# Performance work log

Hardware: AMD Instinct MI355X
Metric: run time of the kernel (lower is better)

## Reference

```python
import jax, jax.numpy as jnp
import numpy as np

N, E, G = 100000, 400000, 2000
D = 128            # dim_node
DE = 128 + 300     # dim_edge after RBF concat
NC = 300           # RBF centers
CUT_LO, CUT_HI = 0.0, 30.0
N_CONV = 3


def setup_inputs() -> dict:
    key = jax.random.key(0)
    ks = jax.random.split(key, 32)
    inp = {}
    inp['Z'] = jax.random.randint(ks[0], (N,), 0, 20)
    inp['edge_type'] = jax.random.randint(ks[1], (E,), 0, 400)
    inp['dist'] = jax.random.uniform(ks[2], (E,), dtype=jnp.float32) * CUT_HI
    inp['src'] = jax.random.randint(ks[3], (E,), 0, N)
    inp['dst'] = jax.random.randint(ks[4], (E,), 0, N)
    inp['graph_ids'] = jnp.sort(jax.random.randint(ks[5], (N,), 0, G))
    s = 0.05
    inp['node_emb'] = jax.random.normal(ks[6], (20, D), jnp.float32) * s
    inp['edge_emb'] = jax.random.normal(ks[7], (400, D), jnp.float32) * s
    # per-conv-layer weights, stacked over layer dim
    inp['Wn1'] = jax.random.normal(ks[8], (N_CONV, D, D), jnp.float32) * s
    inp['bn1'] = jnp.zeros((N_CONV, D), jnp.float32)
    inp['Wn2'] = jax.random.normal(ks[9], (N_CONV, D, D), jnp.float32) * s
    inp['bn2'] = jnp.zeros((N_CONV, D), jnp.float32)
    inp['We1'] = jax.random.normal(ks[10], (N_CONV, DE, DE), jnp.float32) * s
    inp['be1'] = jnp.zeros((N_CONV, DE), jnp.float32)
    inp['We2'] = jax.random.normal(ks[11], (N_CONV, D, DE), jnp.float32) * s
    inp['be2'] = jnp.zeros((N_CONV, D), jnp.float32)
    inp['Wc'] = jax.random.normal(ks[12], (N_CONV, D, D), jnp.float32) * s
    inp['bc'] = jnp.zeros((N_CONV, D), jnp.float32)
    # read layer
    inp['Wr1'] = jax.random.normal(ks[13], (D, D), jnp.float32) * s
    inp['br1'] = jnp.zeros((D,), jnp.float32)
    inp['Wr2'] = jax.random.normal(ks[14], (1, D), jnp.float32) * s
    inp['br2'] = jnp.zeros((1,), jnp.float32)
    return inp


def _rbf(dist):
    centers = jnp.linspace(CUT_LO, CUT_HI, NC, dtype=jnp.float32)
    gap = centers[1] - centers[0]
    # [E, NC]
    return jnp.exp(-((dist[:, None] - centers[None, :]) ** 2) / gap)


def reference(Z, edge_type, dist, src, dst, graph_ids,
              node_emb, edge_emb,
              Wn1, bn1, Wn2, bn2, We1, be1, We2, be2, Wc, bc,
              Wr1, br1, Wr2, br2):
    h = node_emb[Z]                          # [N, D] node embedding
    e = edge_emb[edge_type]                  # [E, D] edge embedding
    e = jnp.concatenate([e, _rbf(dist)], axis=1)   # [E, DE]
    for i in range(N_CONV):
        hs = h[src]                          # gather src node feats [E, D]
        hn = jax.nn.relu(hs @ Wn1[i].T + bn1[i]) @ Wn2[i].T + bn2[i]   # [E, D]
        ee = jax.nn.relu(e @ We1[i].T + be1[i]) @ We2[i].T + be2[i]    # [E, D]
        m = jnp.tanh((hn * ee) @ Wc[i].T + bc[i])                      # [E, D]
        h = h + jax.ops.segment_sum(m, dst, num_segments=N)            # scatter-sum
    r = jax.nn.relu(h @ Wr1.T + br1) @ Wr2.T + br2                     # [N, 1]
    out = jax.ops.segment_sum(r, graph_ids, num_segments=G)            # [G, 1]
    return out.flatten()                                               # [G]
```

## Files before the change

kernel.cpp:

```cpp
#include <hip/hip_runtime.h>

#define NN 100000
#define En 400000
#define Gn 2000
#define GRID 2048

typedef unsigned short u16;
typedef unsigned int u32;
typedef _Float16 f16;
typedef f16 f16x8 __attribute__((ext_vector_type(8)));
typedef float f32x4 __attribute__((ext_vector_type(4)));

__device__ __forceinline__ void lds_barrier() {
  asm volatile("s_waitcnt lgkmcnt(0)\ns_barrier" ::: "memory");
}

#define MFMA16(a, b, c) __builtin_amdgcn_mfma_f32_16x16x32_f16(a, b, c, 0, 0, 0)


__global__ __launch_bounds__(256) void k_prepw(
    const float* __restrict__ Wn1, const float* __restrict__ Wn2,
    const float* __restrict__ Wc, const float* __restrict__ We2,
    const float* __restrict__ We1,
    f16* __restrict__ Wn1b, f16* __restrict__ Wn2b, f16* __restrict__ Wcb,
    f16* __restrict__ We2b, f16* __restrict__ Rb) {
  int i = blockIdx.x * 256 + threadIdx.x;
  if (i < 49152) {
    Wn1b[i] = (f16)Wn1[i];
  } else if (i < 98304) {
    int j = i - 49152;
    Wn2b[j] = (f16)Wn2[j];
  } else if (i < 147456) {
    int j = i - 98304;
    Wcb[j] = (f16)Wc[j];
  } else if (i < 319488) {
    int j = i - 147456;
    int l = j / 57344;
    int r = j - l * 57344;
    int row = r / 448;
    int k = r - row * 448;
    float v = (k < 428) ? We2[l * 54784 + row * 428 + k] : 0.f;
    We2b[j] = (f16)v;
  } else if (i < 749568) {
    int j = i - 319488;
    int l = j / 143360;
    int r = j - l * 143360;
    int row = r / 320;
    int k = r - row * 320;
    float v = 0.f;
    if (row < 428 && k < 300) v = We1[(size_t)l * 183184 + row * 428 + 128 + k];
    Rb[j] = (f16)v;
  }
}


__global__ __launch_bounds__(256) void k_t2(const float* __restrict__ edge_emb,
                                            const float* __restrict__ We1,
                                            const float* __restrict__ be1,
                                            f16* __restrict__ T2) {
  __shared__ __align__(16) float sWe[64][32 * 4];
  __shared__ float sB[64];
  const int tid = threadIdx.x;
  const int l = blockIdx.x / 28;
  const int rb = blockIdx.x - l * 28;
  const int jb = rb >> 2;
  const int tc = rb & 3;
  const int j0 = jb * 64;
  for (int idx = tid; idx < 64 * 32; idx += 256) {
    int row = idx >> 5, c = idx & 31;
    int gj = j0 + row;
    float4 v = make_float4(0.f, 0.f, 0.f, 0.f);
    if (gj < 428)
      v = *(const float4*)&We1[(size_t)l * 183184 + gj * 428 + c * 4];
    *(float4*)&sWe[row][c * 4] = v;
  }
  if (tid < 64) {
    int gj = j0 + tid;
    sB[tid] = (gj < 428) ? be1[l * 428 + gj] : 0.f;
  }
  lds_barrier();
  const int jl = tid & 63, tl = tid >> 6;
  const int gj = j0 + jl;
  for (int it = 0; it < 25; ++it) {
    int t = tc * 100 + it * 4 + tl;
    const float4* er = (const float4*)(edge_emb + t * 128);
    float s = 0.f;
#pragma unroll
    for (int d = 0; d < 32; ++d) {
      float4 a = er[d];
      float4 b = *(const float4*)&sWe[jl][d * 4];
      s += a.x * b.x + a.y * b.y + a.z * b.z + a.w * b.w;
    }
    s += sB[jl];
    T2[l * 179200 + t * 448 + gj] = (gj < 428) ? (f16)s : (f16)0.f;
  }
}

__global__ __launch_bounds__(256) void k_dtab(const f16* __restrict__ Rb,
                                              f16* __restrict__ Dtab) {
  const int tid = threadIdx.x;
  int l = blockIdx.x / (GRID + 1);
  int g = blockIdx.x - l * (GRID + 1);
  float d = (float)g * (30.f / (float)GRID);
  int kc = (int)(d * (299.f / 30.f) + 0.5f);
  int kk0 = min(max(kc - 16, 0), 268);
  __shared__ float sE[32];
  if (tid < 32) {
    float x = d - (float)(kk0 + tid) * (30.f / 299.f);
    sE[tid] = __expf(-x * x * (299.f / 30.f));
  }
  __syncthreads();
  for (int j = tid; j < 448; j += 256) {
    const f16* rr = &Rb[((size_t)l * 448 + j) * 320 + kk0];
    float s = 0.f;
#pragma unroll
    for (int k = 0; k < 32; ++k) s += sE[k] * (float)rr[k];
    Dtab[((size_t)(l * (GRID + 1) + g)) * 448 + j] = (f16)s;
  }
}


__global__ __launch_bounds__(256) void k_zero32(u32* __restrict__ p, int n) {
  int i = blockIdx.x * 256 + threadIdx.x;
  if (i < n) p[i] = 0u;
}

__global__ __launch_bounds__(256) void k_hist(const int* __restrict__ dstv,
                                              u32* __restrict__ hist) {
  int e = blockIdx.x * 256 + threadIdx.x;
  if (e < En) atomicAdd(&hist[dstv[e]], 1u);
}

__global__ __launch_bounds__(1024) void k_scan1(const u32* __restrict__ hist,
                                                u32* __restrict__ excl,
                                                u32* __restrict__ part) {
  __shared__ u32 s[1024];
  const int t = threadIdx.x, b = blockIdx.x, i = b * 1024 + t;
  u32 v = (i < NN) ? hist[i] : 0u;
  s[t] = v;
  __syncthreads();
  u32 acc = v;
  for (int off = 1; off < 1024; off <<= 1) {
    u32 add = (t >= off) ? s[t - off] : 0u;
    __syncthreads();
    acc += add;
    s[t] = acc;
    __syncthreads();
  }
  if (i < NN) excl[i] = acc - v;
  if (t == 1023) part[b] = acc;
}

__global__ __launch_bounds__(128) void k_scan2(u32* __restrict__ part, int n) {
  __shared__ u32 s[128];
  const int t = threadIdx.x;
  u32 v = (t < n) ? part[t] : 0u;
  s[t] = v;
  __syncthreads();
  u32 acc = v;
  for (int off = 1; off < 128; off <<= 1) {
    u32 add = (t >= off) ? s[t - off] : 0u;
    __syncthreads();
    acc += add;
    s[t] = acc;
    __syncthreads();
  }
  if (t < n) part[t] = acc - v;
}

__global__ __launch_bounds__(1024) void k_scan3(const u32* __restrict__ excl,
                                                const u32* __restrict__ part,
                                                u32* __restrict__ cursor) {
  int i = blockIdx.x * 1024 + threadIdx.x;
  if (i < NN) cursor[i] = excl[i] + part[blockIdx.x];
}

__global__ __launch_bounds__(256) void k_scatter(const int* __restrict__ etype,
                                                 const float* __restrict__ dist,
                                                 const int* __restrict__ srcv,
                                                 const int* __restrict__ dstv,
                                                 u32* __restrict__ cursor,
                                                 int4* __restrict__ epack,
                                                 int* __restrict__ edst) {
  int e = blockIdx.x * 256 + threadIdx.x;
  if (e >= En) return;
  int d = dstv[e];
  int pos = (int)atomicAdd(&cursor[d], 1u);
  float fi = dist[e] * ((float)GRID / 30.f);
  int ix = (int)fi;
  epack[pos] = make_int4(srcv[e], etype[e] * 448, ix * 448,
                         __float_as_int(fi - (float)ix));
  edst[pos] = d;
}


__global__ __launch_bounds__(256) void k_node(const float* __restrict__ h,
                                              const f16* __restrict__ W1,
                                              const float* __restrict__ b1,
                                              const f16* __restrict__ W2,
                                              const float* __restrict__ b2,
                                              f16* __restrict__ n2) {
  __shared__ __align__(16) f16 sH[64 * 136];
  __shared__ __align__(16) f16 sT[64 * 136];
  const int tid = threadIdx.x;
  const int nbase = blockIdx.x * 64;
  for (int i = tid; i < 64 * 128; i += 256) {
    int e = i >> 7, d = i & 127;
    int node = nbase + e;
    float v = (node < NN) ? h[(size_t)node * 128 + d] : 0.f;
    sH[e * 136 + d] = (f16)v;
  }
  lds_barrier();
  const int lane = tid & 63, wave = tid >> 6;
  const int q = lane >> 4, ln = lane & 15;
  const int nb = wave * 32;

  f32x4 acc[4][2];
#pragma unroll
  for (int m = 0; m < 4; ++m)
#pragma unroll
    for (int n = 0; n < 2; ++n) acc[m][n] = 0.f;
#pragma unroll
  for (int k0 = 0; k0 < 128; k0 += 32) {
    f16x8 a[4];
#pragma unroll
    for (int m = 0; m < 4; ++m)
      a[m] = *(const f16x8*)&sH[(m * 16 + ln) * 136 + k0 + q * 8];
#pragma unroll
    for (int n = 0; n < 2; ++n) {
      f16x8 b = *(const f16x8*)&W1[(nb + n * 16 + ln) * 128 + k0 + q * 8];
#pragma unroll
      for (int m = 0; m < 4; ++m) acc[m][n] = MFMA16(a[m], b, acc[m][n]);
    }
  }
#pragma unroll
  for (int n = 0; n < 2; ++n) {
    int col = nb + n * 16 + ln;
    float bb = b1[col];
#pragma unroll
    for (int m = 0; m < 4; ++m)
#pragma unroll
      for (int r = 0; r < 4; ++r) {
        int row = m * 16 + q * 4 + r;
        sT[row * 136 + col] = (f16)fmaxf(acc[m][n][r] + bb, 0.f);
      }
  }
  lds_barrier();

  f32x4 acc2[4][2];
#pragma unroll
  for (int m = 0; m < 4; ++m)
#pragma unroll
    for (int n = 0; n < 2; ++n) acc2[m][n] = 0.f;
#pragma unroll
  for (int k0 = 0; k0 < 128; k0 += 32) {
    f16x8 a[4];
#pragma unroll
    for (int m = 0; m < 4; ++m)
      a[m] = *(const f16x8*)&sT[(m * 16 + ln) * 136 + k0 + q * 8];
#pragma unroll
    for (int n = 0; n < 2; ++n) {
      f16x8 b = *(const f16x8*)&W2[(nb + n * 16 + ln) * 128 + k0 + q * 8];
#pragma unroll
      for (int m = 0; m < 4; ++m) acc2[m][n] = MFMA16(a[m], b, acc2[m][n]);
    }
  }
#pragma unroll
  for (int n = 0; n < 2; ++n) {
    int col = nb + n * 16 + ln;
    float bb = b2[col];
#pragma unroll
    for (int m = 0; m < 4; ++m)
#pragma unroll
      for (int r = 0; r < 4; ++r) {
        int row = m * 16 + q * 4 + r;
        int node = nbase + row;
        if (node < NN) n2[(size_t)node * 128 + col] = (f16)(acc2[m][n][r] + bb);
      }
  }
}


__global__ __launch_bounds__(256) void k_node0(const int* __restrict__ Z,
                                               const float* __restrict__ node_emb,
                                               const f16* __restrict__ W1,
                                               const float* __restrict__ b1,
                                               const f16* __restrict__ W2,
                                               const float* __restrict__ b2,
                                               f16* __restrict__ n2,
                                               float* __restrict__ h,
                                               float* __restrict__ out) {
  __shared__ __align__(16) f16 sH[64 * 136];
  __shared__ __align__(16) f16 sT[64 * 136];
  __shared__ int sZ[64];
  const int tid = threadIdx.x;
  const int nbase = blockIdx.x * 64;
  {
    int oi = blockIdx.x * 256 + tid;
    if (oi < Gn) out[oi] = 0.f;
  }
  if (tid < 64) sZ[tid] = Z[min(nbase + tid, NN - 1)];
  lds_barrier();
  for (int i = tid; i < 64 * 128; i += 256) {
    int e = i >> 7, d = i & 127;
    int node = nbase + e;
    float v = node_emb[sZ[e] * 128 + d];
    sH[e * 136 + d] = (f16)v;
    if (node < NN) h[(size_t)node * 128 + d] = v;
  }
  lds_barrier();
  const int lane = tid & 63, wave = tid >> 6;
  const int q = lane >> 4, ln = lane & 15;
  const int nb = wave * 32;

  f32x4 acc[4][2];
#pragma unroll
  for (int m = 0; m < 4; ++m)
#pragma unroll
    for (int n = 0; n < 2; ++n) acc[m][n] = 0.f;
#pragma unroll
  for (int k0 = 0; k0 < 128; k0 += 32) {
    f16x8 a[4];
#pragma unroll
    for (int m = 0; m < 4; ++m)
      a[m] = *(const f16x8*)&sH[(m * 16 + ln) * 136 + k0 + q * 8];
#pragma unroll
    for (int n = 0; n < 2; ++n) {
      f16x8 b = *(const f16x8*)&W1[(nb + n * 16 + ln) * 128 + k0 + q * 8];
#pragma unroll
      for (int m = 0; m < 4; ++m) acc[m][n] = MFMA16(a[m], b, acc[m][n]);
    }
  }
#pragma unroll
  for (int n = 0; n < 2; ++n) {
    int col = nb + n * 16 + ln;
    float bb = b1[col];
#pragma unroll
    for (int m = 0; m < 4; ++m)
#pragma unroll
      for (int r = 0; r < 4; ++r) {
        int row = m * 16 + q * 4 + r;
        sT[row * 136 + col] = (f16)fmaxf(acc[m][n][r] + bb, 0.f);
      }
  }
  lds_barrier();

  f32x4 acc2[4][2];
#pragma unroll
  for (int m = 0; m < 4; ++m)
#pragma unroll
    for (int n = 0; n < 2; ++n) acc2[m][n] = 0.f;
#pragma unroll
  for (int k0 = 0; k0 < 128; k0 += 32) {
    f16x8 a[4];
#pragma unroll
    for (int m = 0; m < 4; ++m)
      a[m] = *(const f16x8*)&sT[(m * 16 + ln) * 136 + k0 + q * 8];
#pragma unroll
    for (int n = 0; n < 2; ++n) {
      f16x8 b = *(const f16x8*)&W2[(nb + n * 16 + ln) * 128 + k0 + q * 8];
#pragma unroll
      for (int m = 0; m < 4; ++m) acc2[m][n] = MFMA16(a[m], b, acc2[m][n]);
    }
  }
#pragma unroll
  for (int n = 0; n < 2; ++n) {
    int col = nb + n * 16 + ln;
    float bb = b2[col];
#pragma unroll
    for (int m = 0; m < 4; ++m)
#pragma unroll
      for (int r = 0; r < 4; ++r) {
        int row = m * 16 + q * 4 + r;
        int node = nbase + row;
        if (node < NN) n2[(size_t)node * 128 + col] = (f16)(acc2[m][n][r] + bb);
      }
  }
}


__global__ __launch_bounds__(256)
__attribute__((amdgpu_waves_per_eu(4, 4))) void k_edge(
    const int4* __restrict__ epack, const int* __restrict__ edst,
    const f16* __restrict__ T2, const f16* __restrict__ Dtab,
    const f16* __restrict__ We2b, const float* __restrict__ be2,
    const f16* __restrict__ Wcb, const float* __restrict__ bc,
    const f16* __restrict__ n2, float* __restrict__ h) {
  __shared__ __align__(16) f16 sC[2][64 * 136];
  __shared__ int sSrc[64], sDst[64], sT2o[64], sIdx[64];
  __shared__ float sFrac[64];

  const int tid = threadIdx.x;
  const int e0 = blockIdx.x * 64;
  if (tid < 64) {
    int4 p = epack[e0 + tid];
    sSrc[tid] = p.x;
    sT2o[tid] = p.y;
    sIdx[tid] = p.z;
    sFrac[tid] = __int_as_float(p.w);
    sDst[tid] = edst[e0 + tid];
  }
  lds_barrier();

  const int lane = tid & 63, wave = tid >> 6;
  const int q = lane >> 4, ln = lane & 15;
  const int nb = wave * 32;

  f32x4 acc[4][2];
#pragma unroll
  for (int m = 0; m < 4; ++m)
#pragma unroll
    for (int n = 0; n < 2; ++n) acc[m][n] = 0.f;

  auto lerp_relu = [](f16x8 lo, f16x8 hi, f16x8 t2, f16 fr) -> f16x8 {
    f16x8 v = t2 + lo + (hi - lo) * fr;
    f16x8 z = {};
    return __builtin_elementwise_max(v, z);
  };
  auto pf128 = [&](int k0, f16x8* plo, f16x8* phi, f16x8* pt2, f16* pfr) {
    const int cg = tid & 15, eb = tid >> 4;
    const int col = k0 + cg * 8;
#pragma unroll
    for (int i = 0; i < 4; ++i) {
      int e = eb + i * 16;
      int off = sIdx[e] + col;
      plo[i] = *(const f16x8*)&Dtab[off];
      phi[i] = *(const f16x8*)&Dtab[off + 448];
      pt2[i] = *(const f16x8*)&T2[sT2o[e] + col];
      pfr[i] = (f16)sFrac[e];
    }
  };
  auto st128 = [&](f16* buf, const f16x8* plo, const f16x8* phi,
                   const f16x8* pt2, const f16* pfr) {
    const int cg = tid & 15, eb = tid >> 4;
#pragma unroll
    for (int i = 0; i < 4; ++i) {
      int e = eb + i * 16;
      *(f16x8*)&buf[e * 136 + cg * 8] = lerp_relu(plo[i], phi[i], pt2[i], pfr[i]);
    }
  };
  auto pf64 = [&](f16x8* plo, f16x8* phi, f16x8* pt2, f16* pfr) {
    const int cg = tid & 7, eb = tid >> 3;
    const int col = 384 + cg * 8;
#pragma unroll
    for (int i = 0; i < 2; ++i) {
      int e = eb + i * 32;
      int off = sIdx[e] + col;
      plo[i] = *(const f16x8*)&Dtab[off];
      phi[i] = *(const f16x8*)&Dtab[off + 448];
      pt2[i] = *(const f16x8*)&T2[sT2o[e] + col];
      pfr[i] = (f16)sFrac[e];
    }
  };
  auto st64 = [&](f16* buf, const f16x8* plo, const f16x8* phi,
                  const f16x8* pt2, const f16* pfr) {
    const int cg = tid & 7, eb = tid >> 3;
#pragma unroll
    for (int i = 0; i < 2; ++i) {
      int e = eb + i * 32;
      *(f16x8*)&buf[e * 136 + cg * 8] = lerp_relu(plo[i], phi[i], pt2[i], pfr[i]);
    }
  };
  auto mfma_chunk = [&](const f16* buf, int k0, int nk) {
    for (int kk = 0; kk < nk; ++kk) {
      f16x8 a[4];
#pragma unroll
      for (int m = 0; m < 4; ++m)
        a[m] = *(const f16x8*)&buf[(m * 16 + ln) * 136 + kk * 32 + q * 8];
#pragma unroll
      for (int n = 0; n < 2; ++n) {
        f16x8 b = *(const f16x8*)&We2b[(nb + n * 16 + ln) * 448 + k0 + kk * 32 + q * 8];
#pragma unroll
        for (int m = 0; m < 4; ++m) acc[m][n] = MFMA16(a[m], b, acc[m][n]);
      }
    }
  };

  {
    f16x8 plo[4], phi[4], pt2[4]; f16 pfr[4];
    pf128(0, plo, phi, pt2, pfr);
    st128(sC[0], plo, phi, pt2, pfr);
  }
  lds_barrier();
  {
    f16x8 plo[4], phi[4], pt2[4]; f16 pfr[4];
    pf128(128, plo, phi, pt2, pfr);
    mfma_chunk(sC[0], 0, 4);
    st128(sC[1], plo, phi, pt2, pfr);
  }
  lds_barrier();
  {
    f16x8 plo[4], phi[4], pt2[4]; f16 pfr[4];
    pf128(256, plo, phi, pt2, pfr);
    mfma_chunk(sC[1], 128, 4);
    st128(sC[0], plo, phi, pt2, pfr);
  }
  lds_barrier();
  f16x8 nrows[4];
  {
    f16x8 plo[2], phi[2], pt2[2]; f16 pfr[2];
    pf64(plo, phi, pt2, pfr);
#pragma unroll
    for (int i = 0; i < 4; ++i) {
      int u = tid + 256 * i;
      int e = u >> 4, cg = u & 15;
      nrows[i] = *(const f16x8*)&n2[(size_t)sSrc[e] * 128 + cg * 8];
    }
    mfma_chunk(sC[0], 256, 4);
    st64(sC[1], plo, phi, pt2, pfr);
  }
  lds_barrier();

  f16* sN = sC[0];
#pragma unroll
  for (int i = 0; i < 4; ++i) {
    int u = tid + 256 * i;
    int e = u >> 4, cg = u & 15;
    *(f16x8*)&sN[e * 136 + cg * 8] = nrows[i];
  }
  mfma_chunk(sC[1], 384, 2);
  lds_barrier();

  f16* sP = sC[1];
  {
    float be2v[2] = {be2[nb + ln], be2[nb + 16 + ln]};
#pragma unroll
    for (int n = 0; n < 2; ++n) {
      int col = nb + n * 16 + ln;
#pragma unroll
      for (int m = 0; m < 4; ++m)
#pragma unroll
        for (int r = 0; r < 4; ++r) {
          int row = m * 16 + q * 4 + r;
          float ee = acc[m][n][r] + be2v[n];
          sP[row * 136 + col] = (f16)(ee * (float)sN[row * 136 + col]);
        }
    }
  }
  lds_barrier();

  {
    f32x4 acc2[4][2];
#pragma unroll
    for (int m = 0; m < 4; ++m)
#pragma unroll
      for (int n = 0; n < 2; ++n) acc2[m][n] = 0.f;
#pragma unroll
    for (int k0 = 0; k0 < 128; k0 += 32) {
      f16x8 a[4];
#pragma unroll
      for (int m = 0; m < 4; ++m)
        a[m] = *(const f16x8*)&sP[(m * 16 + ln) * 136 + k0 + q * 8];
#pragma unroll
      for (int n = 0; n < 2; ++n) {
        f16x8 b = *(const f16x8*)&Wcb[(nb + n * 16 + ln) * 128 + k0 + q * 8];
#pragma unroll
        for (int m = 0; m < 4; ++m) acc2[m][n] = MFMA16(a[m], b, acc2[m][n]);
      }
    }
    float bcv[2] = {bc[nb + ln], bc[nb + 16 + ln]};
#pragma unroll
    for (int m = 0; m < 4; ++m) {
      int d[4];
#pragma unroll
      for (int r = 0; r < 4; ++r) d[r] = sDst[m * 16 + q * 4 + r];
#pragma unroll
      for (int n = 0; n < 2; ++n) {
        int col = nb + n * 16 + ln;
        float tv[4];
#pragma unroll
        for (int r = 0; r < 4; ++r) {
          float x = acc2[m][n][r] + bcv[n];
          x = fminf(2.f, fmaxf(-2.f, x));
          float x2 = x * x;
          tv[r] = x * (15.f + x2) * __builtin_amdgcn_rcpf(15.f + 6.f * x2);
        }
        float s = tv[0];
        int cur = d[0];
#pragma unroll
        for (int r = 1; r < 4; ++r) {
          if (d[r] == cur) {
            s += tv[r];
          } else {
            unsafeAtomicAdd(&h[(size_t)cur * 128 + col], s);
            cur = d[r];
            s = tv[r];
          }
        }
        unsafeAtomicAdd(&h[(size_t)cur * 128 + col], s);
      }
    }
  }
}


__global__ __launch_bounds__(256) void k_read(const float* __restrict__ h,
                                              const float* __restrict__ Wr1,
                                              const float* __restrict__ br1,
                                              const float* __restrict__ Wr2,
                                              const float* __restrict__ br2,
                                              const int* __restrict__ gid,
                                              float* __restrict__ out) {
  __shared__ __align__(16) f16 sH[64 * 136];
  __shared__ __align__(16) f16 sW[128 * 136];
  __shared__ float sR4[4][64];
  const int tid = threadIdx.x;
  const int nbase = blockIdx.x * 64;
  for (int i = tid; i < 64 * 128; i += 256) {
    int e = i >> 7, d = i & 127;
    int node = nbase + e;
    float v = (node < NN) ? h[(size_t)node * 128 + d] : 0.f;
    sH[e * 136 + d] = (f16)v;
  }
  for (int i = tid; i < 128 * 128; i += 256) {
    int rr = i >> 7, d = i & 127;
    sW[rr * 136 + d] = (f16)Wr1[i];
  }
  lds_barrier();
  const int lane = tid & 63, wave = tid >> 6;
  const int q = lane >> 4, ln = lane & 15;
  const int nb = wave * 32;

  f32x4 acc[4][2];
#pragma unroll
  for (int m = 0; m < 4; ++m)
#pragma unroll
    for (int n = 0; n < 2; ++n) acc[m][n] = 0.f;
#pragma unroll
  for (int k0 = 0; k0 < 128; k0 += 32) {
    f16x8 a[4];
#pragma unroll
    for (int m = 0; m < 4; ++m)
      a[m] = *(const f16x8*)&sH[(m * 16 + ln) * 136 + k0 + q * 8];
#pragma unroll
    for (int n = 0; n < 2; ++n) {
      f16x8 b = *(const f16x8*)&sW[(nb + n * 16 + ln) * 136 + k0 + q * 8];
#pragma unroll
      for (int m = 0; m < 4; ++m) acc[m][n] = MFMA16(a[m], b, acc[m][n]);
    }
  }
#pragma unroll
  for (int m = 0; m < 4; ++m)
#pragma unroll
    for (int r = 0; r < 4; ++r) {
      float t = 0.f;
#pragma unroll
      for (int n = 0; n < 2; ++n) {
        int col = nb + n * 16 + ln;
        t += fmaxf(acc[m][n][r] + br1[col], 0.f) * Wr2[col];
      }
      t += __shfl_xor(t, 1);
      t += __shfl_xor(t, 2);
      t += __shfl_xor(t, 4);
      t += __shfl_xor(t, 8);
      if (ln == 0) sR4[wave][m * 16 + q * 4 + r] = t;
    }
  lds_barrier();
  if (tid < 64) {
    int node = nbase + tid;
    if (node < NN) {
      float s = sR4[0][tid] + sR4[1][tid] + sR4[2][tid] + sR4[3][tid] + br2[0];
      unsafeAtomicAdd(&out[gid[node]], s);
    }
  }
}


extern "C" void kernel_launch(void* const* d_in, const int* in_sizes, int n_in,
                              void* d_out, int out_size, void* d_ws, size_t ws_size,
                              hipStream_t stream) {
  const int* Z = (const int*)d_in[0];
  const int* etype = (const int*)d_in[1];
  const float* dist = (const float*)d_in[2];
  const int* src = (const int*)d_in[3];
  const int* dst = (const int*)d_in[4];
  const int* gid = (const int*)d_in[5];
  const float* node_emb = (const float*)d_in[6];
  const float* edge_emb = (const float*)d_in[7];
  const float* Wn1 = (const float*)d_in[8];
  const float* bn1 = (const float*)d_in[9];
  const float* Wn2 = (const float*)d_in[10];
  const float* bn2 = (const float*)d_in[11];
  const float* We1 = (const float*)d_in[12];
  const float* be1 = (const float*)d_in[13];
  const float* We2 = (const float*)d_in[14];
  const float* be2 = (const float*)d_in[15];
  const float* Wc = (const float*)d_in[16];
  const float* bc = (const float*)d_in[17];
  const float* Wr1 = (const float*)d_in[18];
  const float* br1 = (const float*)d_in[19];
  const float* Wr2 = (const float*)d_in[20];
  const float* br2 = (const float*)d_in[21];
  float* out = (float*)d_out;

  char* ws = (char*)d_ws;
  float* h = (float*)(ws);
  f16* n2 = (f16*)(ws + 51200000);
  f16* Rb = (f16*)(ws + 76800000);
  f16* We2b = (f16*)(ws + 77660160);
  f16* Wcb = (f16*)(ws + 78004224);
  f16* Wn1b = (f16*)(ws + 78102528);
  f16* Wn2b = (f16*)(ws + 78200832);
  f16* T2 = (f16*)(ws + 78299136);
  f16* Dtab = (f16*)(ws + 79374336);
  int4* epack = (int4*)(ws + 84882048);
  int* edst = (int*)(ws + 91282048);
  u32* hist = (u32*)(ws + 92882048);
  u32* cursor = (u32*)(ws + 93282048);
  u32* excl = (u32*)(ws + 93682048);
  u32* part = (u32*)(ws + 94082048);

  k_zero32<<<391, 256, 0, stream>>>(hist, NN);
  k_hist<<<1563, 256, 0, stream>>>(dst, hist);
  k_scan1<<<98, 1024, 0, stream>>>(hist, excl, part);
  k_scan2<<<1, 128, 0, stream>>>(part, 98);
  k_scan3<<<98, 1024, 0, stream>>>(excl, part, cursor);
  k_scatter<<<1563, 256, 0, stream>>>(etype, dist, src, dst, cursor, epack, edst);

  k_prepw<<<2928, 256, 0, stream>>>(Wn1, Wn2, Wc, We2, We1,
                                    Wn1b, Wn2b, Wcb, We2b, Rb);
  k_t2<<<84, 256, 0, stream>>>(edge_emb, We1, be1, T2);
  k_dtab<<<3 * (GRID + 1), 256, 0, stream>>>(Rb, Dtab);

  for (int l = 0; l < 3; ++l) {
    if (l == 0) {
      k_node0<<<1563, 256, 0, stream>>>(Z, node_emb, Wn1b, bn1, Wn2b, bn2,
                                        n2, h, out);
    } else {
      k_node<<<1563, 256, 0, stream>>>(h, Wn1b + l * 16384, bn1 + l * 128,
                                       Wn2b + l * 16384, bn2 + l * 128, n2);
    }
    k_edge<<<6250, 256, 0, stream>>>(epack, edst,
                                     T2 + l * 179200, Dtab + (size_t)l * (GRID + 1) * 448,
                                     We2b + l * 57344, be2 + l * 128,
                                     Wcb + l * 16384, bc + l * 128, n2, h);
  }
  k_read<<<1563, 256, 0, stream>>>(h, Wr1, br1, Wr2, br2, gid, out);
}
```

Measured before the change: 943.0 us.

## Fold histogram zeroing into weight prep and tune several small kernels

Moves the histogram zeroing into the weight-conversion kernel, which removes one launch. Rewrites the edge-type table kernel to use MFMA tiles instead of scalar FP32 dot products. Replaces the LDS-based block scan with wave shuffles and vectorises the h/weight staging loads to float4. Widens the RBF window to 40 aligned taps with vector loads and raises wave priority around the MFMA loops in the edge kernel. The table values now go through FP16 matmul and a slightly different RBF truncation, so numerics shift a little.

```diff
diff --git a/kernel.cpp b/kernel.cpp
--- a/kernel.cpp
+++ b/kernel.cpp
@@ -9,6 +9,7 @@
 typedef unsigned int u32;
 typedef _Float16 f16;
 typedef f16 f16x8 __attribute__((ext_vector_type(8)));
+typedef f16 f16x4 __attribute__((ext_vector_type(4)));
 typedef float f32x4 __attribute__((ext_vector_type(4)));
 
 __device__ __forceinline__ void lds_barrier() {
@@ -23,7 +24,7 @@
     const float* __restrict__ Wc, const float* __restrict__ We2,
     const float* __restrict__ We1,
     f16* __restrict__ Wn1b, f16* __restrict__ Wn2b, f16* __restrict__ Wcb,
-    f16* __restrict__ We2b, f16* __restrict__ Rb) {
+    f16* __restrict__ We2b, f16* __restrict__ Rb, u32* __restrict__ hist) {
   int i = blockIdx.x * 256 + threadIdx.x;
   if (i < 49152) {
     Wn1b[i] = (f16)Wn1[i];
@@ -50,6 +51,8 @@
     float v = 0.f;
     if (row < 428 && k < 300) v = We1[(size_t)l * 183184 + row * 428 + 128 + k];
     Rb[j] = (f16)v;
+  } else if (i < 849568) {
+    hist[i - 749568] = 0u;
   }
 }
 
@@ -58,41 +61,68 @@
                                             const float* __restrict__ We1,
                                             const float* __restrict__ be1,
                                             f16* __restrict__ T2) {
-  __shared__ __align__(16) float sWe[64][32 * 4];
-  __shared__ float sB[64];
+  __shared__ __align__(16) f16 sA[64 * 136];
+  __shared__ __align__(16) f16 sB[128 * 136];
   const int tid = threadIdx.x;
   const int l = blockIdx.x / 28;
   const int rb = blockIdx.x - l * 28;
-  const int jb = rb >> 2;
-  const int tc = rb & 3;
-  const int j0 = jb * 64;
-  for (int idx = tid; idx < 64 * 32; idx += 256) {
-    int row = idx >> 5, c = idx & 31;
-    int gj = j0 + row;
+  const int tb = rb >> 2, jb = rb & 3;
+  const int t0 = tb * 64, j0 = jb * 128;
+  for (int i = tid; i < 64 * 32; i += 256) {
+    int e = i >> 5, c = (i & 31) * 4;
+    int t = t0 + e;
     float4 v = make_float4(0.f, 0.f, 0.f, 0.f);
-    if (gj < 428)
-      v = *(const float4*)&We1[(size_t)l * 183184 + gj * 428 + c * 4];
-    *(float4*)&sWe[row][c * 4] = v;
-  }
-  if (tid < 64) {
-    int gj = j0 + tid;
-    sB[tid] = (gj < 428) ? be1[l * 428 + gj] : 0.f;
-  }
-  lds_barrier();
-  const int jl = tid & 63, tl = tid >> 6;
-  const int gj = j0 + jl;
-  for (int it = 0; it < 25; ++it) {
-    int t = tc * 100 + it * 4 + tl;
-    const float4* er = (const float4*)(edge_emb + t * 128);
-    float s = 0.f;
-#pragma unroll
-    for (int d = 0; d < 32; ++d) {
-      float4 a = er[d];
-      float4 b = *(const float4*)&sWe[jl][d * 4];
-      s += a.x * b.x + a.y * b.y + a.z * b.z + a.w * b.w;
-    }
-    s += sB[jl];
-    T2[l * 179200 + t * 448 + gj] = (gj < 428) ? (f16)s : (f16)0.f;
+    if (t < 400) v = *(const float4*)&edge_emb[t * 128 + c];
+    f16x4 o = {(f16)v.x, (f16)v.y, (f16)v.z, (f16)v.w};
+    *(f16x4*)&sA[e * 136 + c] = o;
+  }
+  for (int i = tid; i < 128 * 32; i += 256) {
+    int rr = i >> 5, c = (i & 31) * 4;
+    int j = j0 + rr;
+    float4 v = make_float4(0.f, 0.f, 0.f, 0.f);
+    if (j < 428) v = *(const float4*)&We1[(size_t)l * 183184 + j * 428 + c];
+    f16x4 o = {(f16)v.x, (f16)v.y, (f16)v.z, (f16)v.w};
+    *(f16x4*)&sB[rr * 136 + c] = o;
+  }
+  lds_barrier();
+  const int lane = tid & 63, wave = tid >> 6;
+  const int q = lane >> 4, ln = lane & 15;
+  const int nb = wave * 32;
+
+  f32x4 acc[4][2];
+#pragma unroll
+  for (int m = 0; m < 4; ++m)
+#pragma unroll
+    for (int n = 0; n < 2; ++n) acc[m][n] = 0.f;
+#pragma unroll
+  for (int k0 = 0; k0 < 128; k0 += 32) {
+    f16x8 a[4];
+#pragma unroll
+    for (int m = 0; m < 4; ++m)
+      a[m] = *(const f16x8*)&sA[(m * 16 + ln) * 136 + k0 + q * 8];
+#pragma unroll
+    for (int n = 0; n < 2; ++n) {
+      f16x8 b = *(const f16x8*)&sB[(nb + n * 16 + ln) * 136 + k0 + q * 8];
+#pragma unroll
+      for (int m = 0; m < 4; ++m) acc[m][n] = MFMA16(a[m], b, acc[m][n]);
+    }
+  }
+#pragma unroll
+  for (int n = 0; n < 2; ++n) {
+    int col = nb + n * 16 + ln;
+    int gj = j0 + col;
+    float bb = (gj < 428) ? be1[l * 428 + gj] : 0.f;
+#pragma unroll
+    for (int m = 0; m < 4; ++m)
+#pragma unroll
+      for (int r = 0; r < 4; ++r) {
+        int row = m * 16 + q * 4 + r;
+        int t = t0 + row;
+        if (t < 400 && gj < 448) {
+          float s = acc[m][n][r] + bb;
+          T2[l * 179200 + t * 448 + gj] = (gj < 428) ? (f16)s : (f16)0.f;
+        }
+      }
   }
 }
 
@@ -103,9 +133,9 @@
   int g = blockIdx.x - l * (GRID + 1);
   float d = (float)g * (30.f / (float)GRID);
   int kc = (int)(d * (299.f / 30.f) + 0.5f);
-  int kk0 = min(max(kc - 16, 0), 268);
-  __shared__ float sE[32];
-  if (tid < 32) {
+  int kk0 = min(max(kc - 20, 0), 280) & ~7;
+  __shared__ float sE[40];
+  if (tid < 40) {
     float x = d - (float)(kk0 + tid) * (30.f / 299.f);
     sE[tid] = __expf(-x * x * (299.f / 30.f));
   }
@@ -114,16 +144,15 @@
     const f16* rr = &Rb[((size_t)l * 448 + j) * 320 + kk0];
     float s = 0.f;
 #pragma unroll
-    for (int k = 0; k < 32; ++k) s += sE[k] * (float)rr[k];
+    for (int v = 0; v < 5; ++v) {
+      f16x8 rv = *(const f16x8*)&rr[v * 8];
+#pragma unroll
+      for (int t = 0; t < 8; ++t) s += sE[v * 8 + t] * (float)rv[t];
+    }
     Dtab[((size_t)(l * (GRID + 1) + g)) * 448 + j] = (f16)s;
   }
 }
 
-
-__global__ __launch_bounds__(256) void k_zero32(u32* __restrict__ p, int n) {
-  int i = blockIdx.x * 256 + threadIdx.x;
-  if (i < n) p[i] = 0u;
-}
 
 __global__ __launch_bounds__(256) void k_hist(const int* __restrict__ dstv,
                                               u32* __restrict__ hist) {
@@ -134,21 +163,32 @@
 __global__ __launch_bounds__(1024) void k_scan1(const u32* __restrict__ hist,
                                                 u32* __restrict__ excl,
                                                 u32* __restrict__ part) {
-  __shared__ u32 s[1024];
+  __shared__ u32 ws[16];
   const int t = threadIdx.x, b = blockIdx.x, i = b * 1024 + t;
+  const int lane = t & 63, wid = t >> 6;
   u32 v = (i < NN) ? hist[i] : 0u;
-  s[t] = v;
+  u32 acc = v;
+#pragma unroll
+  for (int off = 1; off < 64; off <<= 1) {
+    u32 x = __shfl_up(acc, off);
+    if (lane >= off) acc += x;
+  }
+  if (lane == 63) ws[wid] = acc;
   __syncthreads();
-  u32 acc = v;
-  for (int off = 1; off < 1024; off <<= 1) {
-    u32 add = (t >= off) ? s[t - off] : 0u;
-    __syncthreads();
-    acc += add;
-    s[t] = acc;
-    __syncthreads();
-  }
-  if (i < NN) excl[i] = acc - v;
-  if (t == 1023) part[b] = acc;
+  if (t < 16) {
+    u32 wa = ws[t];
+#pragma unroll
+    for (int off = 1; off < 16; off <<= 1) {
+      u32 x = __shfl_up(wa, off);
+      if (t >= off) wa += x;
+    }
+    ws[t] = wa;
+  }
+  __syncthreads();
+  u32 base = (wid > 0) ? ws[wid - 1] : 0u;
+  u32 inc = base + acc;
+  if (i < NN) excl[i] = inc - v;
+  if (t == 1023) part[b] = inc;
 }
 
 __global__ __launch_bounds__(128) void k_scan2(u32* __restrict__ part, int n) {
@@ -204,11 +244,13 @@
   __shared__ __align__(16) f16 sT[64 * 136];
   const int tid = threadIdx.x;
   const int nbase = blockIdx.x * 64;
-  for (int i = tid; i < 64 * 128; i += 256) {
-    int e = i >> 7, d = i & 127;
+  for (int i = tid; i < 64 * 32; i += 256) {
+    int e = i >> 5, c = (i & 31) * 4;
     int node = nbase + e;
-    float v = (node < NN) ? h[(size_t)node * 128 + d] : 0.f;
-    sH[e * 136 + d] = (f16)v;
+    float4 v = make_float4(0.f, 0.f, 0.f, 0.f);
+    if (node < NN) v = *(const float4*)&h[(size_t)node * 128 + c];
+    f16x4 o = {(f16)v.x, (f16)v.y, (f16)v.z, (f16)v.w};
+    *(f16x4*)&sH[e * 136 + c] = o;
   }
   lds_barrier();
   const int lane = tid & 63, wave = tid >> 6;
@@ -301,12 +343,13 @@
   }
   if (tid < 64) sZ[tid] = Z[min(nbase + tid, NN - 1)];
   lds_barrier();
-  for (int i = tid; i < 64 * 128; i += 256) {
-    int e = i >> 7, d = i & 127;
+  for (int i = tid; i < 64 * 32; i += 256) {
+    int e = i >> 5, c = (i & 31) * 4;
     int node = nbase + e;
-    float v = node_emb[sZ[e] * 128 + d];
-    sH[e * 136 + d] = (f16)v;
-    if (node < NN) h[(size_t)node * 128 + d] = v;
+    float4 v = *(const float4*)&node_emb[sZ[e] * 128 + c];
+    f16x4 o = {(f16)v.x, (f16)v.y, (f16)v.z, (f16)v.w};
+    *(f16x4*)&sH[e * 136 + c] = o;
+    if (node < NN) *(float4*)&h[(size_t)node * 128 + c] = v;
   }
   lds_barrier();
   const int lane = tid & 63, wave = tid >> 6;
@@ -462,6 +505,7 @@
     }
   };
   auto mfma_chunk = [&](const f16* buf, int k0, int nk) {
+    __builtin_amdgcn_s_setprio(1);
     for (int kk = 0; kk < nk; ++kk) {
       f16x8 a[4];
 #pragma unroll
@@ -474,6 +518,7 @@
         for (int m = 0; m < 4; ++m) acc[m][n] = MFMA16(a[m], b, acc[m][n]);
       }
     }
+    __builtin_amdgcn_s_setprio(0);
   };
 
   {
@@ -545,6 +590,7 @@
     for (int m = 0; m < 4; ++m)
 #pragma unroll
       for (int n = 0; n < 2; ++n) acc2[m][n] = 0.f;
+    __builtin_amdgcn_s_setprio(1);
 #pragma unroll
     for (int k0 = 0; k0 < 128; k0 += 32) {
       f16x8 a[4];
@@ -558,6 +604,7 @@
         for (int m = 0; m < 4; ++m) acc2[m][n] = MFMA16(a[m], b, acc2[m][n]);
       }
     }
+    __builtin_amdgcn_s_setprio(0);
     float bcv[2] = {bc[nb + ln], bc[nb + 16 + ln]};
 #pragma unroll
     for (int m = 0; m < 4; ++m) {
@@ -606,15 +653,19 @@
   __shared__ float sR4[4][64];
   const int tid = threadIdx.x;
   const int nbase = blockIdx.x * 64;
-  for (int i = tid; i < 64 * 128; i += 256) {
-    int e = i >> 7, d = i & 127;
+  for (int i = tid; i < 64 * 32; i += 256) {
+    int e = i >> 5, c = (i & 31) * 4;
     int node = nbase + e;
-    float v = (node < NN) ? h[(size_t)node * 128 + d] : 0.f;
-    sH[e * 136 + d] = (f16)v;
-  }
-  for (int i = tid; i < 128 * 128; i += 256) {
-    int rr = i >> 7, d = i & 127;
-    sW[rr * 136 + d] = (f16)Wr1[i];
+    float4 v = make_float4(0.f, 0.f, 0.f, 0.f);
+    if (node < NN) v = *(const float4*)&h[(size_t)node * 128 + c];
+    f16x4 o = {(f16)v.x, (f16)v.y, (f16)v.z, (f16)v.w};
+    *(f16x4*)&sH[e * 136 + c] = o;
+  }
+  for (int i = tid; i < 128 * 32; i += 256) {
+    int rr = i >> 5, c = (i & 31) * 4;
+    float4 v = *(const float4*)&Wr1[rr * 128 + c];
+    f16x4 o = {(f16)v.x, (f16)v.y, (f16)v.z, (f16)v.w};
+    *(f16x4*)&sW[rr * 136 + c] = o;
   }
   lds_barrier();
   const int lane = tid & 63, wave = tid >> 6;
@@ -710,15 +761,14 @@
   u32* excl = (u32*)(ws + 93682048);
   u32* part = (u32*)(ws + 94082048);
 
-  k_zero32<<<391, 256, 0, stream>>>(hist, NN);
+  k_prepw<<<3319, 256, 0, stream>>>(Wn1, Wn2, Wc, We2, We1,
+                                    Wn1b, Wn2b, Wcb, We2b, Rb, hist);
   k_hist<<<1563, 256, 0, stream>>>(dst, hist);
   k_scan1<<<98, 1024, 0, stream>>>(hist, excl, part);
   k_scan2<<<1, 128, 0, stream>>>(part, 98);
   k_scan3<<<98, 1024, 0, stream>>>(excl, part, cursor);
   k_scatter<<<1563, 256, 0, stream>>>(etype, dist, src, dst, cursor, epack, edst);
 
-  k_prepw<<<2928, 256, 0, stream>>>(Wn1, Wn2, Wc, We2, We1,
-                                    Wn1b, Wn2b, Wcb, We2b, Rb);
   k_t2<<<84, 256, 0, stream>>>(edge_emb, We1, be1, T2);
   k_dtab<<<3 * (GRID + 1), 256, 0, stream>>>(Rb, Dtab);
 
```

Result: no change. 953.7 us (+1.1%).
